# Kernel optimization log

Measured on AMD Instinct MI355X. Metric: run time of the kernel, lower is better.

The kernel has to match this reference:

```python
import jax, jax.numpy as jnp
import numpy as np

N = 100000   # nodes
F = 64       # features
K = 5        # filter taps
E = 1600000  # edges per sparse power (avg degree 16)


def setup_inputs() -> dict:
    key = jax.random.key(0)
    k1, k2, k3, k4, k5 = jax.random.split(key, 5)
    x = jax.random.normal(k1, (N, F), dtype=jnp.float32)
    h = jax.random.normal(k2, (K,), dtype=jnp.float32)
    vals = jax.random.normal(k3, (K, E), dtype=jnp.float32)
    rows = jax.random.randint(k4, (K, E), 0, N, dtype=jnp.int32)
    cols = jax.random.randint(k5, (K, E), 0, N, dtype=jnp.int32)
    return {"x": x, "h": h, "vals": vals, "rows": rows, "cols": cols}


def reference(x, h, vals, rows, cols):
    # H = sum_k h[k] * S_k  (COO);  out = H @ x
    # Fuse the weighted sum of K sparse matrices directly into one SpMM:
    # scale each power's values by h[k], flatten all K edge lists, and
    # scatter-add the gathered rows of x.
    n = x.shape[0]
    w = (h[:, None] * vals).reshape(-1)          # [K*E]
    r = rows.reshape(-1)                         # [K*E]
    c = cols.reshape(-1)                         # [K*E]
    contrib = x[c] * w[:, None]                  # [K*E, F] gather + scale
    out = jax.ops.segment_sum(contrib, r, num_segments=n)  # [N, F]
    return out
```

## Files before the change

kernel.cpp:

```cpp
#include <hip/hip_runtime.h>


#define RPB   64
#define SUB   2
#define GWG   128

static __global__ __launch_bounds__(1024) void count_kernel(
    const int* __restrict__ rows, int* __restrict__ cnt,
    int KE, int NSTREAM, int chunk)
{
    extern __shared__ int hist[];
    const int g = blockIdx.x;
    for (int j = threadIdx.x; j < NSTREAM; j += blockDim.x) hist[j] = 0;
    __syncthreads();
    const int lo = g * chunk;
    const int hi = min(lo + chunk, KE);
    for (int e = lo + threadIdx.x; e < hi; e += blockDim.x) {
        const int r = rows[e];
        atomicAdd(&hist[((r >> 6) << 1) | (r & 1)], 1);
    }
    __syncthreads();
    for (int j = threadIdx.x; j < NSTREAM; j += blockDim.x)
        cnt[(size_t)j * GWG + g] = hist[j];
}

static __global__ __launch_bounds__(GWG) void scan1_kernel(
    int* __restrict__ cnt, int* __restrict__ ssBeg)
{
    __shared__ int tmp[GWG];
    const int s = blockIdx.x;
    const int t = threadIdx.x;
    const int v = cnt[(size_t)s * GWG + t];
    tmp[t] = v;
    __syncthreads();
    for (int d = 1; d < GWG; d <<= 1) {
        int u = (t >= d) ? tmp[t - d] : 0;
        __syncthreads();
        tmp[t] += u;
        __syncthreads();
    }
    cnt[(size_t)s * GWG + t] = tmp[t] - v;
    if (t == GWG - 1) ssBeg[s] = tmp[t];
}

static __global__ __launch_bounds__(1024) void scan2_kernel(
    int* __restrict__ a, int n)
{
    __shared__ int sums[1024];
    const int t = threadIdx.x;
    const int chunk = (n + 1023) >> 10;
    const int lo = t * chunk;
    const int hi = min(lo + chunk, n);
    int s = 0;
    for (int i = lo; i < hi; ++i) s += a[i];
    sums[t] = s;
    __syncthreads();
    for (int d = 1; d < 1024; d <<= 1) {
        int v = (t >= d) ? sums[t - d] : 0;
        __syncthreads();
        sums[t] += v;
        __syncthreads();
    }
    int run = (t > 0) ? sums[t - 1] : 0;
    for (int i = lo; i < hi; ++i) {
        const int cv = a[i];
        a[i] = run;
        run += cv;
    }
    if (t == 1023) a[n] = sums[1023];
}

static __global__ __launch_bounds__(1024) void scan3_kernel(
    int* __restrict__ cnt, const int* __restrict__ ssBeg, int total)
{
    const int i = blockIdx.x * blockDim.x + threadIdx.x;
    if (i < total) cnt[i] += ssBeg[i >> 7];
}

static __global__ __launch_bounds__(1024) void scatter_kernel(
    const int*   __restrict__ rows,
    const int*   __restrict__ cols,
    const float* __restrict__ vals,
    const float* __restrict__ h,
    const int*   __restrict__ cnt,
    int2*        __restrict__ payload,
    int KE, int E, int K, int NSTREAM, int chunk)
{
    extern __shared__ int lcur[];
    const int g = blockIdx.x;
    for (int j = threadIdx.x; j < NSTREAM; j += blockDim.x)
        lcur[j] = cnt[(size_t)j * GWG + g];
    __syncthreads();
    const int lo = g * chunk;
    const int hi = min(lo + chunk, KE);
    if (lo >= hi) return;
    const int k0 = lo / E;
    const int k1 = min((hi - 1) / E, K - 1);
    for (int k = k0; k <= k1; ++k) {
        const float hk = h[k];
        const int s0 = max(lo, k * E);
        const int s1 = min(hi, (k + 1) * E);
        for (int e = s0 + threadIdx.x; e < s1; e += blockDim.x) {
            const int r = rows[e];
            const int st = ((r >> 6) << 1) | (r & 1);
            const int pos = atomicAdd(&lcur[st], 1);
            payload[pos] = make_int2(((r & 63) << 17) | cols[e],
                                     __float_as_int(hk * vals[e]));
        }
    }
}

static __global__ __launch_bounds__(128) void spmv_kernel(
    const int*  __restrict__ ssBeg,
    const int2* __restrict__ payload,
    const float* __restrict__ x,
    float*       __restrict__ out,
    int N)
{
    __shared__ float acc[RPB * 64];
    const int b = blockIdx.x;
    for (int i = threadIdx.x; i < RPB * 64; i += 128) acc[i] = 0.f;
    __syncthreads();

    const int lane = threadIdx.x & 63;
    const int wv   = threadIdx.x >> 6;
    const int s    = b * SUB + wv;
    int e        = ssBeg[s];
    const int be = ssBeg[s + 1];

    while (e + 16 <= be) {
        int2 pa[8], pb[8];
        float xa[8], xb[8];
        #pragma unroll
        for (int j = 0; j < 8; ++j) pa[j] = payload[e + j];
        #pragma unroll
        for (int j = 0; j < 8; ++j) pb[j] = payload[e + 8 + j];
        #pragma unroll
        for (int j = 0; j < 8; ++j)
            xa[j] = x[(size_t)(pa[j].x & 0x1FFFF) * 64 + lane];
        #pragma unroll
        for (int j = 0; j < 8; ++j)
            xb[j] = x[(size_t)(pb[j].x & 0x1FFFF) * 64 + lane];
        #pragma unroll
        for (int j = 0; j < 8; ++j)
            acc[(pa[j].x >> 17) * 64 + lane] += __int_as_float(pa[j].y) * xa[j];
        #pragma unroll
        for (int j = 0; j < 8; ++j)
            acc[(pb[j].x >> 17) * 64 + lane] += __int_as_float(pb[j].y) * xb[j];
        e += 16;
    }
    for (; e < be; ++e) {
        const int2 p = payload[e];
        acc[(p.x >> 17) * 64 + lane] +=
            __int_as_float(p.y) * x[(size_t)(p.x & 0x1FFFF) * 64 + lane];
    }
    __syncthreads();

    const int base = b * RPB;
    const int nrow = min(RPB, N - base);
    for (int i = threadIdx.x; i < nrow * 64; i += 128)
        out[(size_t)base * 64 + i] = acc[i];
}

static __global__ __launch_bounds__(256) void gtconv_scatter(
    const float* __restrict__ x, const float* __restrict__ h,
    const float* __restrict__ vals, const int* __restrict__ rows,
    const int* __restrict__ cols, float* __restrict__ out, int KE, int E)
{
    const int lane = threadIdx.x & 63;
    int wave = (blockIdx.x * blockDim.x + threadIdx.x) >> 6;
    const int nwaves = (gridDim.x * blockDim.x) >> 6;
    for (int e = wave; e < KE; e += nwaves) {
        float w = h[e / E] * vals[e];
        float xv = x[(size_t)cols[e] * 64 + lane];
        unsafeAtomicAdd(&out[(size_t)rows[e] * 64 + lane], xv * w);
    }
}

extern "C" void kernel_launch(void* const* d_in, const int* in_sizes, int n_in,
                              void* d_out, int out_size, void* d_ws, size_t ws_size,
                              hipStream_t stream) {
    const float* x    = (const float*)d_in[0];
    const float* h    = (const float*)d_in[1];
    const float* vals = (const float*)d_in[2];
    const int*   rows = (const int*)d_in[3];
    const int*   cols = (const int*)d_in[4];
    float* out = (float*)d_out;

    const int K  = in_sizes[1];
    const int KE = in_sizes[2];
    const int E  = KE / K;
    const int F  = 64;
    const int N  = in_sizes[0] / F;
    const int NB      = (N + RPB - 1) / RPB;
    const int NSTREAM = NB * SUB;

    const size_t lds_need = (size_t)NSTREAM * 4;
    const size_t cnt_off  = 0;
    const size_t cnt_sz   = (size_t)NSTREAM * GWG * 4;
    const size_t ss_off   = cnt_off + cnt_sz;
    const size_t ss_sz    = (size_t)(NSTREAM + 1) * 4;
    const size_t pl_off   = (ss_off + ss_sz + 15) & ~(size_t)15;
    const size_t need     = pl_off + (size_t)KE * 8;

    if (ws_size < need || lds_need > 64 * 1024) {
        hipMemsetAsync(out, 0, (size_t)out_size * sizeof(float), stream);
        gtconv_scatter<<<8192, 256, 0, stream>>>(x, h, vals, rows, cols, out, KE, E);
        return;
    }

    char* ws = (char*)d_ws;
    int*  cnt     = (int*)(ws + cnt_off);
    int*  ssBeg   = (int*)(ws + ss_off);
    int2* payload = (int2*)(ws + pl_off);

    const int chunk = (KE + GWG - 1) / GWG;

    count_kernel<<<GWG, 1024, lds_need, stream>>>(rows, cnt, KE, NSTREAM, chunk);
    scan1_kernel<<<NSTREAM, GWG, 0, stream>>>(cnt, ssBeg);
    scan2_kernel<<<1, 1024, 0, stream>>>(ssBeg, NSTREAM);
    const int total = NSTREAM * GWG;
    scan3_kernel<<<(total + 1023) / 1024, 1024, 0, stream>>>(cnt, ssBeg, total);
    scatter_kernel<<<GWG, 1024, lds_need, stream>>>(rows, cols, vals, h, cnt,
                                                    payload, KE, E, K, NSTREAM, chunk);
    spmv_kernel<<<NB, 128, 0, stream>>>(ssBeg, payload, x, out, N);
}
```

Measured before the change: 407.6 us.

## Process two row streams per wave with half-wave float2 gathers in SpMV

The SpMV kernel now has each half-wave gather one edge's x row with 8-byte float2 loads. As a result, one wave instruction covers two edges, one from each of the block's two row streams. Each stream's edge range is split in half between the two waves. Each wave accumulates into its own LDS copy, and the two copies are summed at write-out. This is meant to double the edges in flight per memory instruction and balance the uneven stream lengths across waves. The costs are doubled LDS per block, which may lower occupancy, and serial leftover loops where half the lanes sit idle.

```diff
diff --git a/kernel.cpp b/kernel.cpp
--- a/kernel.cpp
+++ b/kernel.cpp
@@ -117,49 +117,97 @@
     float*       __restrict__ out,
     int N)
 {
-    __shared__ float acc[RPB * 64];
-    const int b = blockIdx.x;
-    for (int i = threadIdx.x; i < RPB * 64; i += 128) acc[i] = 0.f;
-    __syncthreads();
-
-    const int lane = threadIdx.x & 63;
-    const int wv   = threadIdx.x >> 6;
-    const int s    = b * SUB + wv;
-    int e        = ssBeg[s];
-    const int be = ssBeg[s + 1];
-
-    while (e + 16 <= be) {
-        int2 pa[8], pb[8];
-        float xa[8], xb[8];
+    __shared__ float2 acc[2][RPB * 32];
+    const int tid = threadIdx.x;
+    for (int i = tid; i < RPB * 32; i += 128) {
+        acc[0][i] = make_float2(0.f, 0.f);
+        acc[1][i] = make_float2(0.f, 0.f);
+    }
+    __syncthreads();
+
+    const int b    = blockIdx.x;
+    const int lane = tid & 63;
+    const int wv   = tid >> 6;
+    const int m    = lane & 31;
+    const int hl   = lane >> 5;
+    const float2* xp = (const float2*)x;
+    float2* ac = acc[wv];
+
+    const int l0 = ssBeg[2 * b];
+    const int r0 = ssBeg[2 * b + 1];
+    const int r1 = ssBeg[2 * b + 2];
+    const int n0 = r0 - l0, n1 = r1 - r0;
+    const int h0 = n0 >> 1, h1 = n1 >> 1;
+    const int a0 = l0 + h0 * wv, b0 = wv ? r0 : (l0 + h0);
+    const int a1 = r0 + h1 * wv, b1 = wv ? r1 : (r0 + h1);
+    const int len0 = b0 - a0, len1 = b1 - a1;
+    const int np = min(len0, len1);
+    const int base = hl ? a1 : a0;
+
+    int j = 0;
+    while (j + 8 <= np) {
+        int2 pp[8];
+        float2 xx[8];
         #pragma unroll
-        for (int j = 0; j < 8; ++j) pa[j] = payload[e + j];
+        for (int q = 0; q < 8; ++q) pp[q] = payload[base + j + q];
         #pragma unroll
-        for (int j = 0; j < 8; ++j) pb[j] = payload[e + 8 + j];
+        for (int q = 0; q < 8; ++q)
+            xx[q] = xp[(size_t)(pp[q].x & 0x1FFFF) * 32 + m];
         #pragma unroll
-        for (int j = 0; j < 8; ++j)
-            xa[j] = x[(size_t)(pa[j].x & 0x1FFFF) * 64 + lane];
-        #pragma unroll
-        for (int j = 0; j < 8; ++j)
-            xb[j] = x[(size_t)(pb[j].x & 0x1FFFF) * 64 + lane];
-        #pragma unroll
-        for (int j = 0; j < 8; ++j)
-            acc[(pa[j].x >> 17) * 64 + lane] += __int_as_float(pa[j].y) * xa[j];
-        #pragma unroll
-        for (int j = 0; j < 8; ++j)
-            acc[(pb[j].x >> 17) * 64 + lane] += __int_as_float(pb[j].y) * xb[j];
-        e += 16;
-    }
-    for (; e < be; ++e) {
-        const int2 p = payload[e];
-        acc[(p.x >> 17) * 64 + lane] +=
-            __int_as_float(p.y) * x[(size_t)(p.x & 0x1FFFF) * 64 + lane];
-    }
-    __syncthreads();
-
-    const int base = b * RPB;
-    const int nrow = min(RPB, N - base);
-    for (int i = threadIdx.x; i < nrow * 64; i += 128)
-        out[(size_t)base * 64 + i] = acc[i];
+        for (int q = 0; q < 8; ++q) {
+            const float w  = __int_as_float(pp[q].y);
+            const int   rl = pp[q].x >> 17;
+            float2 cur = ac[rl * 32 + m];
+            cur.x += w * xx[q].x;
+            cur.y += w * xx[q].y;
+            ac[rl * 32 + m] = cur;
+        }
+        j += 8;
+    }
+    for (; j < np; ++j) {
+        const int2 p = payload[base + j];
+        const float2 xv = xp[(size_t)(p.x & 0x1FFFF) * 32 + m];
+        const float w  = __int_as_float(p.y);
+        const int   rl = p.x >> 17;
+        float2 cur = ac[rl * 32 + m];
+        cur.x += w * xv.x;
+        cur.y += w * xv.y;
+        ac[rl * 32 + m] = cur;
+    }
+    for (int t = a0 + np; t < b0; ++t) {
+        const int2 p = payload[t];
+        const float2 xv = xp[(size_t)(p.x & 0x1FFFF) * 32 + m];
+        if (hl == 0) {
+            const float w  = __int_as_float(p.y);
+            const int   rl = p.x >> 17;
+            float2 cur = ac[rl * 32 + m];
+            cur.x += w * xv.x;
+            cur.y += w * xv.y;
+            ac[rl * 32 + m] = cur;
+        }
+    }
+    for (int t = a1 + np; t < b1; ++t) {
+        const int2 p = payload[t];
+        const float2 xv = xp[(size_t)(p.x & 0x1FFFF) * 32 + m];
+        if (hl == 0) {
+            const float w  = __int_as_float(p.y);
+            const int   rl = p.x >> 17;
+            float2 cur = ac[rl * 32 + m];
+            cur.x += w * xv.x;
+            cur.y += w * xv.y;
+            ac[rl * 32 + m] = cur;
+        }
+    }
+    __syncthreads();
+
+    const int basev = b * RPB;
+    const int nrow = min(RPB, N - basev);
+    float2* op = (float2*)(out + (size_t)basev * 64);
+    for (int i = tid; i < nrow * 32; i += 128) {
+        const float2 u = acc[0][i];
+        const float2 v = acc[1][i];
+        op[i] = make_float2(u.x + v.x, u.y + v.y);
+    }
 }
 
 static __global__ __launch_bounds__(256) void gtconv_scatter(
```

Measured after the change: 513.6 us. +26.0%, slower.

## Use bf16 features and weights, partition counters globally, and merge scan kernels

Applied to the files above, without the earlier changes.

Converts x to a bf16 copy and stores edge weights as bf16 in a split index/weight payload. This halves the gather and payload traffic in the SpMM. The per-workgroup count matrix and three-stage scan are replaced by 8 partitioned global counters, filled with atomics and scanned by a single kernel. The scatter now uses global atomics on those partitioned cursors. This loses precision in x and the weights, and adds a conversion pass plus contention on the global atomics.

```diff
diff --git a/kernel.cpp b/kernel.cpp
--- a/kernel.cpp
+++ b/kernel.cpp
@@ -1,16 +1,19 @@
 #include <hip/hip_runtime.h>
-
-
-#define RPB   64
-#define SUB   2
-#define GWG   128
+#include <hip/hip_bf16.h>
+
+
+#define RPB    64
+#define SUB    2
+#define NPART  8
+#define GWG    1024
 
 static __global__ __launch_bounds__(1024) void count_kernel(
     const int* __restrict__ rows, int* __restrict__ cnt,
-    int KE, int NSTREAM, int chunk)
+    int KE, int NSTREAM, int PS, int chunk)
 {
     extern __shared__ int hist[];
     const int g = blockIdx.x;
+    const int p = g & (NPART - 1);
     for (int j = threadIdx.x; j < NSTREAM; j += blockDim.x) hist[j] = 0;
     __syncthreads();
     const int lo = g * chunk;
@@ -20,39 +23,25 @@
         atomicAdd(&hist[((r >> 6) << 1) | (r & 1)], 1);
     }
     __syncthreads();
-    for (int j = threadIdx.x; j < NSTREAM; j += blockDim.x)
-        cnt[(size_t)j * GWG + g] = hist[j];
-}
-
-static __global__ __launch_bounds__(GWG) void scan1_kernel(
-    int* __restrict__ cnt, int* __restrict__ ssBeg)
-{
-    __shared__ int tmp[GWG];
-    const int s = blockIdx.x;
-    const int t = threadIdx.x;
-    const int v = cnt[(size_t)s * GWG + t];
-    tmp[t] = v;
-    __syncthreads();
-    for (int d = 1; d < GWG; d <<= 1) {
-        int u = (t >= d) ? tmp[t - d] : 0;
-        __syncthreads();
-        tmp[t] += u;
-        __syncthreads();
-    }
-    cnt[(size_t)s * GWG + t] = tmp[t] - v;
-    if (t == GWG - 1) ssBeg[s] = tmp[t];
-}
-
-static __global__ __launch_bounds__(1024) void scan2_kernel(
-    int* __restrict__ a, int n)
+    for (int j = threadIdx.x; j < NSTREAM; j += blockDim.x) {
+        const int v = hist[j];
+        if (v) atomicAdd(&cnt[p * PS + j], v);
+    }
+}
+
+static __global__ __launch_bounds__(1024) void scan_kernel(
+    const int* __restrict__ cnt, int* __restrict__ ssBeg8,
+    int* __restrict__ cur, int NSTREAM, int PS)
 {
     __shared__ int sums[1024];
+    const int n = NSTREAM * NPART;
     const int t = threadIdx.x;
     const int chunk = (n + 1023) >> 10;
     const int lo = t * chunk;
     const int hi = min(lo + chunk, n);
     int s = 0;
-    for (int i = lo; i < hi; ++i) s += a[i];
+    for (int i = lo; i < hi; ++i)
+        s += cnt[(i & (NPART - 1)) * PS + (i >> 3)];
     sums[t] = s;
     __syncthreads();
     for (int d = 1; d < 1024; d <<= 1) {
@@ -63,34 +52,28 @@
     }
     int run = (t > 0) ? sums[t - 1] : 0;
     for (int i = lo; i < hi; ++i) {
-        const int cv = a[i];
-        a[i] = run;
+        const int phys = (i & (NPART - 1)) * PS + (i >> 3);
+        const int cv = cnt[phys];
+        ssBeg8[i] = run;
+        cur[phys] = run;
         run += cv;
     }
-    if (t == 1023) a[n] = sums[1023];
-}
-
-static __global__ __launch_bounds__(1024) void scan3_kernel(
-    int* __restrict__ cnt, const int* __restrict__ ssBeg, int total)
-{
-    const int i = blockIdx.x * blockDim.x + threadIdx.x;
-    if (i < total) cnt[i] += ssBeg[i >> 7];
-}
-
-static __global__ __launch_bounds__(1024) void scatter_kernel(
+    if (t == 1023) ssBeg8[n] = sums[1023];
+}
+
+static __global__ __launch_bounds__(256) void scatter_kernel(
     const int*   __restrict__ rows,
     const int*   __restrict__ cols,
     const float* __restrict__ vals,
     const float* __restrict__ h,
-    const int*   __restrict__ cnt,
-    int2*        __restrict__ payload,
-    int KE, int E, int K, int NSTREAM, int chunk)
-{
-    extern __shared__ int lcur[];
+    int*         __restrict__ cur,
+    int*         __restrict__ pidx,
+    ushort*      __restrict__ pw,
+    int KE, int E, int K, int PS, int chunk)
+{
     const int g = blockIdx.x;
-    for (int j = threadIdx.x; j < NSTREAM; j += blockDim.x)
-        lcur[j] = cnt[(size_t)j * GWG + g];
-    __syncthreads();
+    const int p = g & (NPART - 1);
+    int* mycur = cur + (size_t)p * PS;
     const int lo = g * chunk;
     const int hi = min(lo + chunk, KE);
     if (lo >= hi) return;
@@ -103,18 +86,33 @@
         for (int e = s0 + threadIdx.x; e < s1; e += blockDim.x) {
             const int r = rows[e];
             const int st = ((r >> 6) << 1) | (r & 1);
-            const int pos = atomicAdd(&lcur[st], 1);
-            payload[pos] = make_int2(((r & 63) << 17) | cols[e],
-                                     __float_as_int(hk * vals[e]));
+            const int pos = atomicAdd(&mycur[st], 1);
+            pidx[pos] = ((r & 63) << 17) | cols[e];
+            pw[pos] = __bfloat16_as_ushort(__float2bfloat16(hk * vals[e]));
         }
     }
 }
 
+static __global__ __launch_bounds__(256) void convert_kernel(
+    const float* __restrict__ x, ushort* __restrict__ xh, int n4)
+{
+    const int i = blockIdx.x * blockDim.x + threadIdx.x;
+    if (i >= n4) return;
+    const float4 v = ((const float4*)x)[i];
+    ushort4 o;
+    o.x = __bfloat16_as_ushort(__float2bfloat16(v.x));
+    o.y = __bfloat16_as_ushort(__float2bfloat16(v.y));
+    o.z = __bfloat16_as_ushort(__float2bfloat16(v.z));
+    o.w = __bfloat16_as_ushort(__float2bfloat16(v.w));
+    ((ushort4*)xh)[i] = o;
+}
+
 static __global__ __launch_bounds__(128) void spmv_kernel(
-    const int*  __restrict__ ssBeg,
-    const int2* __restrict__ payload,
-    const float* __restrict__ x,
-    float*       __restrict__ out,
+    const int*    __restrict__ ssBeg8,
+    const int*    __restrict__ pidx,
+    const ushort* __restrict__ pw,
+    const ushort* __restrict__ xh,
+    float*        __restrict__ out,
     int N)
 {
     __shared__ float acc[RPB * 64];
@@ -125,34 +123,41 @@
     const int lane = threadIdx.x & 63;
     const int wv   = threadIdx.x >> 6;
     const int s    = b * SUB + wv;
-    int e        = ssBeg[s];
-    const int be = ssBeg[s + 1];
+    int e        = ssBeg8[(size_t)s * NPART];
+    const int be = ssBeg8[(size_t)(s + 1) * NPART];
 
     while (e + 16 <= be) {
-        int2 pa[8], pb[8];
+        int ia[8], ib[8];
+        ushort wa[8], wb[8];
         float xa[8], xb[8];
         #pragma unroll
-        for (int j = 0; j < 8; ++j) pa[j] = payload[e + j];
-        #pragma unroll
-        for (int j = 0; j < 8; ++j) pb[j] = payload[e + 8 + j];
-        #pragma unroll
-        for (int j = 0; j < 8; ++j)
-            xa[j] = x[(size_t)(pa[j].x & 0x1FFFF) * 64 + lane];
-        #pragma unroll
-        for (int j = 0; j < 8; ++j)
-            xb[j] = x[(size_t)(pb[j].x & 0x1FFFF) * 64 + lane];
-        #pragma unroll
-        for (int j = 0; j < 8; ++j)
-            acc[(pa[j].x >> 17) * 64 + lane] += __int_as_float(pa[j].y) * xa[j];
-        #pragma unroll
-        for (int j = 0; j < 8; ++j)
-            acc[(pb[j].x >> 17) * 64 + lane] += __int_as_float(pb[j].y) * xb[j];
+        for (int j = 0; j < 8; ++j) { ia[j] = pidx[e + j]; wa[j] = pw[e + j]; }
+        #pragma unroll
+        for (int j = 0; j < 8; ++j) { ib[j] = pidx[e + 8 + j]; wb[j] = pw[e + 8 + j]; }
+        #pragma unroll
+        for (int j = 0; j < 8; ++j)
+            xa[j] = __bfloat162float(__ushort_as_bfloat16(
+                        xh[(size_t)(ia[j] & 0x1FFFF) * 64 + lane]));
+        #pragma unroll
+        for (int j = 0; j < 8; ++j)
+            xb[j] = __bfloat162float(__ushort_as_bfloat16(
+                        xh[(size_t)(ib[j] & 0x1FFFF) * 64 + lane]));
+        #pragma unroll
+        for (int j = 0; j < 8; ++j)
+            acc[(ia[j] >> 17) * 64 + lane] +=
+                __bfloat162float(__ushort_as_bfloat16(wa[j])) * xa[j];
+        #pragma unroll
+        for (int j = 0; j < 8; ++j)
+            acc[(ib[j] >> 17) * 64 + lane] +=
+                __bfloat162float(__ushort_as_bfloat16(wb[j])) * xb[j];
         e += 16;
     }
     for (; e < be; ++e) {
-        const int2 p = payload[e];
-        acc[(p.x >> 17) * 64 + lane] +=
-            __int_as_float(p.y) * x[(size_t)(p.x & 0x1FFFF) * 64 + lane];
+        const int i_ = pidx[e];
+        const float xv = __bfloat162float(__ushort_as_bfloat16(
+                             xh[(size_t)(i_ & 0x1FFFF) * 64 + lane]));
+        acc[(i_ >> 17) * 64 + lane] +=
+            __bfloat162float(__ushort_as_bfloat16(pw[e])) * xv;
     }
     __syncthreads();
 
@@ -194,14 +199,18 @@
     const int N  = in_sizes[0] / F;
     const int NB      = (N + RPB - 1) / RPB;
     const int NSTREAM = NB * SUB;
+    const int PS      = (NSTREAM + 15) & ~15;
 
     const size_t lds_need = (size_t)NSTREAM * 4;
     const size_t cnt_off  = 0;
-    const size_t cnt_sz   = (size_t)NSTREAM * GWG * 4;
-    const size_t ss_off   = cnt_off + cnt_sz;
-    const size_t ss_sz    = (size_t)(NSTREAM + 1) * 4;
-    const size_t pl_off   = (ss_off + ss_sz + 15) & ~(size_t)15;
-    const size_t need     = pl_off + (size_t)KE * 8;
+    const size_t cnt_sz   = (size_t)NPART * PS * 4;
+    const size_t cur_off  = cnt_off + cnt_sz;
+    const size_t ss_off   = cur_off + cnt_sz;
+    const size_t ss_sz    = ((size_t)NSTREAM * NPART + 1) * 4;
+    const size_t pi_off   = (ss_off + ss_sz + 63) & ~(size_t)63;
+    const size_t pw_off   = pi_off + (size_t)KE * 4;
+    const size_t xh_off   = (pw_off + (size_t)KE * 2 + 63) & ~(size_t)63;
+    const size_t need     = xh_off + (size_t)N * F * 2;
 
     if (ws_size < need || lds_need > 64 * 1024) {
         hipMemsetAsync(out, 0, (size_t)out_size * sizeof(float), stream);
@@ -210,18 +219,21 @@
     }
 
     char* ws = (char*)d_ws;
-    int*  cnt     = (int*)(ws + cnt_off);
-    int*  ssBeg   = (int*)(ws + ss_off);
-    int2* payload = (int2*)(ws + pl_off);
+    int*    cnt    = (int*)(ws + cnt_off);
+    int*    cur    = (int*)(ws + cur_off);
+    int*    ssBeg8 = (int*)(ws + ss_off);
+    int*    pidx   = (int*)(ws + pi_off);
+    ushort* pw     = (ushort*)(ws + pw_off);
+    ushort* xh     = (ushort*)(ws + xh_off);
+
+    hipMemsetAsync(cnt, 0, cnt_sz, stream);
+    const int n4 = (N * F) / 4;
+    convert_kernel<<<(n4 + 255) / 256, 256, 0, stream>>>(x, xh, n4);
 
     const int chunk = (KE + GWG - 1) / GWG;
-
-    count_kernel<<<GWG, 1024, lds_need, stream>>>(rows, cnt, KE, NSTREAM, chunk);
-    scan1_kernel<<<NSTREAM, GWG, 0, stream>>>(cnt, ssBeg);
-    scan2_kernel<<<1, 1024, 0, stream>>>(ssBeg, NSTREAM);
-    const int total = NSTREAM * GWG;
-    scan3_kernel<<<(total + 1023) / 1024, 1024, 0, stream>>>(cnt, ssBeg, total);
-    scatter_kernel<<<GWG, 1024, lds_need, stream>>>(rows, cols, vals, h, cnt,
-                                                    payload, KE, E, K, NSTREAM, chunk);
-    spmv_kernel<<<NB, 128, 0, stream>>>(ssBeg, payload, x, out, N);
-}
+    count_kernel<<<GWG, 1024, lds_need, stream>>>(rows, cnt, KE, NSTREAM, PS, chunk);
+    scan_kernel<<<1, 1024, 0, stream>>>(cnt, ssBeg8, cur, NSTREAM, PS);
+    scatter_kernel<<<GWG, 256, 0, stream>>>(rows, cols, vals, h, cur,
+                                            pidx, pw, KE, E, K, PS, chunk);
+    spmv_kernel<<<NB, 128, 0, stream>>>(ssBeg8, pidx, pw, xh, out, N);
+}
```

Result: slower. 722.0 us (+77.1%).
